# Kernel tuning notes

Measured on AMD Instinct MI355X. Metric: run time of the kernel, lower is better.

The kernel has to match this reference:

```python
import jax, jax.numpy as jnp
import numpy as np

SCALE = 1.0 / np.sqrt(7.0)  # window_size ** 0.5 with window_size=7


def setup_inputs() -> dict:
    key = jax.random.key(0)
    ks = jax.random.split(key, 7)
    B, C, H, W = 8, 64, 64, 64
    O = 64
    x = jax.random.normal(ks[0], (B, C, H, W), dtype=jnp.float32)
    s = 1.0 / np.sqrt(C)
    Wq = jax.random.normal(ks[1], (O, C), dtype=jnp.float32) * s
    bq = jax.random.normal(ks[2], (O,), dtype=jnp.float32) * 0.01
    Wk = jax.random.normal(ks[3], (O, C), dtype=jnp.float32) * s
    bk = jax.random.normal(ks[4], (O,), dtype=jnp.float32) * 0.01
    Wv = jax.random.normal(ks[5], (O, C), dtype=jnp.float32) * s
    bv = jax.random.normal(ks[6], (O,), dtype=jnp.float32) * 0.01
    return {"x": x, "Wq": Wq, "bq": bq, "Wk": Wk, "bk": bk, "Wv": Wv, "bv": bv}


def reference(x, Wq, bq, Wk, bk, Wv, bv):
    B, C, H, W = x.shape
    O = Wq.shape[0]
    N = H * W
    # 1x1 convs == per-pixel linear projections
    xf = x.reshape(B, C, N)  # [B, C, N]
    q = jnp.einsum('bcn,oc->bon', xf, Wq) + bq[None, :, None]  # [B, O, N]
    k = jnp.einsum('bcn,oc->bon', xf, Wk) + bk[None, :, None]
    v = jnp.einsum('bcn,oc->bon', xf, Wv) + bv[None, :, None]
    # global attention over all H*W positions
    attn = jnp.einsum('bcn,bcm->bnm', q, k) * SCALE  # [B, N, N]
    attn = jax.nn.softmax(attn, axis=-1)
    out = jnp.einsum('bnm,bcm->bnc', attn, v)  # [B, N, O]
    # faithful to torch's out.view(B, -1, H, W): raw row-major reshape of [B, N, O]
    return out.reshape(B, O, H, W)
```

## Files before the change

### kernel.cpp

```cpp
#include <hip/hip_runtime.h>
#include <math.h>

#define B_ 8
#define N_ 4096
#define SCALE2_ 0.54528747f

typedef __bf16 bf16x8 __attribute__((ext_vector_type(8)));
typedef float f32x4 __attribute__((ext_vector_type(4)));
typedef float f32x16 __attribute__((ext_vector_type(16)));
typedef unsigned short ushortx8 __attribute__((ext_vector_type(8)));
typedef unsigned short ushort;
typedef unsigned int uint;
typedef uint uint2v __attribute__((ext_vector_type(2)));

static __device__ __forceinline__ ushort f2bf(float f) {
  union { float f; unsigned u; } v; v.f = f;
  unsigned r = v.u + 0x7FFFu + ((v.u >> 16) & 1u);
  return (ushort)(r >> 16);
}
static __device__ __forceinline__ uint pk2(float a, float b) {
  union { __bf16 h[2]; uint u; } v;
  v.h[0] = (__bf16)a; v.h[1] = (__bf16)b;
  return v.u;
}

__global__ __launch_bounds__(256)
void proj_kernel(const float* __restrict__ x,
                 const float* __restrict__ Wq, const float* __restrict__ bq,
                 const float* __restrict__ Wk, const float* __restrict__ bk,
                 const float* __restrict__ Wv, const float* __restrict__ bv,
                 ushort* __restrict__ Qb, ushort* __restrict__ KF,
                 ushort* __restrict__ VF)
{
  __shared__ ushort sm[256][17];

  const int tid = threadIdx.x;
  const int gp  = (blockIdx.x << 8) + tid;
  const int b   = gp >> 12;
  const int y   = blockIdx.y;
  const int mat = y >> 2;
  const int o0  = (y & 3) << 4;
  const int n   = gp & 4095;

  const float* xb = x + ((size_t)b << 18) + n;
  float xr[64];
  #pragma unroll
  for (int c = 0; c < 64; ++c) xr[c] = xb[(size_t)c << 12];

  const float* W    = (mat == 0) ? Wq : (mat == 1) ? Wk : Wv;
  const float* bias = (mat == 0) ? bq : (mat == 1) ? bk : bv;

  float acc[16];
  #pragma unroll 1
  for (int j = 0; j < 16; ++j) {
    const float4* wr = (const float4*)(W + ((o0 + j) << 6));
    float a = bias[o0 + j];
    #pragma unroll
    for (int c4 = 0; c4 < 16; ++c4) {
      float4 w4 = wr[c4];
      a += w4.x * xr[4*c4] + w4.y * xr[4*c4+1] + w4.z * xr[4*c4+2] + w4.w * xr[4*c4+3];
    }
    acc[j] = a;
  }

  if (mat == 2) {
    #pragma unroll
    for (int j = 0; j < 16; ++j) sm[tid][j] = f2bf(acc[j]);
    __syncthreads();
    const int ol   = tid & 15;
    const int hh   = (tid >> 4) & 1;
    const int kvbl = tid >> 5;
    const int nb   = (blockIdx.x << 8) & 4095;
    const int kvblk = (nb >> 5) + kvbl;
    #pragma unroll
    for (int ks2 = 0; ks2 < 2; ++ks2) {
      const int kvl = (kvbl << 5) + (ks2 << 4) + (hh << 3);
      uint pk[4];
      #pragma unroll
      for (int cj = 0; cj < 8; ++cj) {
        ushort v = sm[kvl + cj][ol];
        if (cj & 1) pk[cj >> 1] |= (uint)v << 16; else pk[cj >> 1] = v;
      }
      const size_t A = ((size_t)(b * 128 + kvblk)) * 2048 + (ks2 << 10)
                     + (hh << 9) + ((o0 + ol) << 3);
      *(ushortx8*)(VF + A) = *(ushortx8*)&pk[0];
    }
  } else if (mat == 1) {
    const int ks = y & 3;
    __align__(16) ushort hv[16];
    #pragma unroll
    for (int j = 0; j < 16; ++j) hv[j] = f2bf(acc[j]);
    const size_t A0 = ((size_t)(b * 128 + (n >> 5))) * 2048 + (ks << 9)
                    + ((n & 31) << 3);
    *(ushortx8*)(KF + A0)       = *(const ushortx8*)&hv[0];
    *(ushortx8*)(KF + A0 + 256) = *(const ushortx8*)&hv[8];
  } else {
    __align__(16) ushort hv[16];
    #pragma unroll
    for (int j = 0; j < 16; ++j) hv[j] = f2bf(acc[j] * SCALE2_);
    const size_t base = ((size_t)gp << 6) + o0;
    *(ushortx8*)(Qb + base)     = *(const ushortx8*)&hv[0];
    *(ushortx8*)(Qb + base + 8) = *(const ushortx8*)&hv[8];
  }
}

__global__ __launch_bounds__(256, 3)
void flash_kernel(const ushort* __restrict__ Qb, const ushort* __restrict__ KF,
                  const ushort* __restrict__ VF, float* __restrict__ out)
{
  __shared__ float cmb[3][64][33];

  const int tid  = threadIdx.x;
  const int lane = tid & 63;
  const int w    = tid >> 6;
  const int r32  = lane & 31;
  const int h    = lane >> 5;
  const int h8   = h << 3;

  const int bidx = (blockIdx.x & 7) * 128 + (blockIdx.x >> 3);
  const int b  = bidx >> 7;
  const int qw = (bidx & 127) << 5;

  bf16x8 qf[4];
  {
    const ushort* qp = Qb + ((((size_t)b << 12) + qw + r32) << 6) + h8;
    #pragma unroll
    for (int ks = 0; ks < 4; ++ks) qf[ks] = *(const bf16x8*)(qp + (ks << 4));
  }

  const ushort* kb = KF + ((size_t)((b << 7) + (w << 5))) * 2048 + (lane << 3);
  const ushort* vb = VF + ((size_t)((b << 7) + (w << 5))) * 2048 + (h << 9) + (r32 << 3);

  const f32x16 Z = (f32x16)(0.0f);
  f32x16 acc0 = Z, acc1 = Z;
  float l_lane = 0.f;

  bf16x8 kA[4], vA[4], kB[4], vB[4];
  #define LDK(D, P) do { \
    D[0] = *(const bf16x8*)(P); \
    D[1] = *(const bf16x8*)((P) + 512); \
    D[2] = *(const bf16x8*)((P) + 1024); \
    D[3] = *(const bf16x8*)((P) + 1536); \
  } while (0)
  #define LDV(D, P) do { \
    D[0] = *(const bf16x8*)(P); \
    D[1] = *(const bf16x8*)((P) + 256); \
    D[2] = *(const bf16x8*)((P) + 1024); \
    D[3] = *(const bf16x8*)((P) + 1280); \
  } while (0)

  #define COMPUTE(KFr, VFr) do { \
    __builtin_amdgcn_s_setprio(1); \
    f32x16 s = __builtin_amdgcn_mfma_f32_32x32x16_bf16(KFr[0], qf[0], Z, 0, 0, 0); \
    s = __builtin_amdgcn_mfma_f32_32x32x16_bf16(KFr[1], qf[1], s, 0, 0, 0); \
    s = __builtin_amdgcn_mfma_f32_32x32x16_bf16(KFr[2], qf[2], s, 0, 0, 0); \
    s = __builtin_amdgcn_mfma_f32_32x32x16_bf16(KFr[3], qf[3], s, 0, 0, 0); \
    __builtin_amdgcn_s_setprio(0); \
    float rs = 0.f; \
    _Pragma("unroll") \
    for (int ii = 0; ii < 16; ++ii) { \
      float p = __builtin_exp2f(s[ii]); \
      s[ii] = p; \
      rs += p; \
    } \
    l_lane += rs; \
    bf16x8 pb0, pb1; \
    { \
      uint plo0 = pk2(s[0], s[1]); \
      uint plo1 = pk2(s[2], s[3]); \
      uint phi0 = pk2(s[4], s[5]); \
      uint phi1 = pk2(s[6], s[7]); \
      uint2v r0 = __builtin_amdgcn_permlane32_swap(plo0, phi0, false, false); \
      uint2v r1 = __builtin_amdgcn_permlane32_swap(plo1, phi1, false, false); \
      union { uint u[4]; bf16x8 v; } f_; \
      f_.u[0] = r0.x; f_.u[1] = r1.x; f_.u[2] = r0.y; f_.u[3] = r1.y; \
      pb0 = f_.v; \
    } \
    { \
      uint plo0 = pk2(s[8],  s[9]); \
      uint plo1 = pk2(s[10], s[11]); \
      uint phi0 = pk2(s[12], s[13]); \
      uint phi1 = pk2(s[14], s[15]); \
      uint2v r0 = __builtin_amdgcn_permlane32_swap(plo0, phi0, false, false); \
      uint2v r1 = __builtin_amdgcn_permlane32_swap(plo1, phi1, false, false); \
      union { uint u[4]; bf16x8 v; } f_; \
      f_.u[0] = r0.x; f_.u[1] = r1.x; f_.u[2] = r0.y; f_.u[3] = r1.y; \
      pb1 = f_.v; \
    } \
    __builtin_amdgcn_s_setprio(1); \
    acc0 = __builtin_amdgcn_mfma_f32_32x32x16_bf16(VFr[0], pb0, acc0, 0, 0, 0); \
    acc1 = __builtin_amdgcn_mfma_f32_32x32x16_bf16(VFr[1], pb0, acc1, 0, 0, 0); \
    acc0 = __builtin_amdgcn_mfma_f32_32x32x16_bf16(VFr[2], pb1, acc0, 0, 0, 0); \
    acc1 = __builtin_amdgcn_mfma_f32_32x32x16_bf16(VFr[3], pb1, acc1, 0, 0, 0); \
    __builtin_amdgcn_s_setprio(0); \
  } while (0)

  LDK(kA, kb); LDV(vA, vb);
  #pragma unroll 1
  for (int t = 0; t < 16; ++t) {
    kb += 2048; vb += 2048;
    LDK(kB, kb); LDV(vB, vb);
    COMPUTE(kA, vA);
    kb += 2048; vb += 2048;
    LDK(kA, kb); LDV(vA, vb);
    COMPUTE(kB, vB);
  }

  float l_me = l_lane + __shfl_xor(l_lane, 32);

  if (w != 0) {
    float* p = &cmb[w - 1][lane][0];
    #pragma unroll
    for (int i = 0; i < 16; ++i) { p[i] = acc0[i]; p[16 + i] = acc1[i]; }
    p[32] = l_me;
  }
  __syncthreads();
  if (w == 0) {
    float lsum = l_me;
    #pragma unroll
    for (int q = 0; q < 3; ++q) lsum += cmb[q][lane][32];
    const float inv = 1.0f / lsum;
    const size_t rowb = (((size_t)b << 12) + qw + r32) << 6;
    #pragma unroll
    for (int g = 0; g < 4; ++g) {
      f32x4 o4;
      #pragma unroll
      for (int i = 0; i < 4; ++i) {
        float v = acc0[4*g + i];
        #pragma unroll
        for (int q = 0; q < 3; ++q) v += cmb[q][lane][4*g + i];
        o4[i] = v * inv;
      }
      *(f32x4*)(out + rowb + (g << 3) + (h << 2)) = o4;
    }
    #pragma unroll
    for (int g = 0; g < 4; ++g) {
      f32x4 o4;
      #pragma unroll
      for (int i = 0; i < 4; ++i) {
        float v = acc1[4*g + i];
        #pragma unroll
        for (int q = 0; q < 3; ++q) v += cmb[q][lane][16 + 4*g + i];
        o4[i] = v * inv;
      }
      *(f32x4*)(out + rowb + 32 + (g << 3) + (h << 2)) = o4;
    }
  }
  #undef LDK
  #undef LDV
  #undef COMPUTE
}

extern "C" void kernel_launch(void* const* d_in, const int* in_sizes, int n_in,
                              void* d_out, int out_size, void* d_ws, size_t ws_size,
                              hipStream_t stream) {
  (void)in_sizes; (void)n_in; (void)out_size; (void)ws_size;
  const float* x  = (const float*)d_in[0];
  const float* Wq = (const float*)d_in[1];
  const float* bq = (const float*)d_in[2];
  const float* Wk = (const float*)d_in[3];
  const float* bk = (const float*)d_in[4];
  const float* Wv = (const float*)d_in[5];
  const float* bv = (const float*)d_in[6];
  float* out = (float*)d_out;

  const size_t SZ = (size_t)B_ * N_ * 64;
  ushort* Qb = (ushort*)d_ws;
  ushort* KF = Qb + SZ;
  ushort* VF = KF + SZ;

  proj_kernel<<<dim3(128, 12), dim3(256), 0, stream>>>(x, Wq, bq, Wk, bk, Wv, bv,
                                                       Qb, KF, VF);
  flash_kernel<<<dim3(1024), dim3(256), 0, stream>>>(Qb, KF, VF, out);
}
```

Baseline: 82.88 us.

## Process two 32-row query tiles per block to reuse K/V loads

Each flash block now handles 64 query rows (two 32-row tiles) instead of 32, so each K/V fragment loaded from global memory feeds two QK^T and PV tile computations. The grid halves to 512 blocks, occupancy target drops to 2 blocks per CU, and the combine buffer in shared memory doubles. The explicit double-buffered K/V prefetch is removed in favor of loading at the top of each iteration and relying on the two tiles' compute to hide latency. This risks exposed load latency and lower parallelism, traded for halved K/V traffic.

```diff
diff --git a/kernel.cpp b/kernel.cpp
--- a/kernel.cpp
+++ b/kernel.cpp
@@ -104,11 +104,11 @@
   }
 }
 
-__global__ __launch_bounds__(256, 3)
+__global__ __launch_bounds__(256, 2)
 void flash_kernel(const ushort* __restrict__ Qb, const ushort* __restrict__ KF,
                   const ushort* __restrict__ VF, float* __restrict__ out)
 {
-  __shared__ float cmb[3][64][33];
+  __shared__ float cmb[3][64][66];
 
   const int tid  = threadIdx.x;
   const int lane = tid & 63;
@@ -117,44 +117,34 @@
   const int h    = lane >> 5;
   const int h8   = h << 3;
 
-  const int bidx = (blockIdx.x & 7) * 128 + (blockIdx.x >> 3);
-  const int b  = bidx >> 7;
-  const int qw = (bidx & 127) << 5;
-
-  bf16x8 qf[4];
+  const int bidx = (blockIdx.x & 7) * 64 + (blockIdx.x >> 3);
+  const int b  = bidx >> 6;
+  const int qw = (bidx & 63) << 6;
+
+  bf16x8 qfA[4], qfB[4];
   {
-    const ushort* qp = Qb + ((((size_t)b << 12) + qw + r32) << 6) + h8;
-    #pragma unroll
-    for (int ks = 0; ks < 4; ++ks) qf[ks] = *(const bf16x8*)(qp + (ks << 4));
+    const ushort* qa = Qb + ((((size_t)b << 12) + qw + r32) << 6) + h8;
+    const ushort* qb2 = Qb + ((((size_t)b << 12) + qw + 32 + r32) << 6) + h8;
+    #pragma unroll
+    for (int ks = 0; ks < 4; ++ks) {
+      qfA[ks] = *(const bf16x8*)(qa + (ks << 4));
+      qfB[ks] = *(const bf16x8*)(qb2 + (ks << 4));
+    }
   }
 
   const ushort* kb = KF + ((size_t)((b << 7) + (w << 5))) * 2048 + (lane << 3);
   const ushort* vb = VF + ((size_t)((b << 7) + (w << 5))) * 2048 + (h << 9) + (r32 << 3);
 
   const f32x16 Z = (f32x16)(0.0f);
-  f32x16 acc0 = Z, acc1 = Z;
-  float l_lane = 0.f;
-
-  bf16x8 kA[4], vA[4], kB[4], vB[4];
-  #define LDK(D, P) do { \
-    D[0] = *(const bf16x8*)(P); \
-    D[1] = *(const bf16x8*)((P) + 512); \
-    D[2] = *(const bf16x8*)((P) + 1024); \
-    D[3] = *(const bf16x8*)((P) + 1536); \
-  } while (0)
-  #define LDV(D, P) do { \
-    D[0] = *(const bf16x8*)(P); \
-    D[1] = *(const bf16x8*)((P) + 256); \
-    D[2] = *(const bf16x8*)((P) + 1024); \
-    D[3] = *(const bf16x8*)((P) + 1280); \
-  } while (0)
-
-  #define COMPUTE(KFr, VFr) do { \
+  f32x16 accA0 = Z, accA1 = Z, accB0 = Z, accB1 = Z;
+  float lA = 0.f, lB = 0.f;
+
+  #define TILE(QF, A0, A1, LV) do { \
     __builtin_amdgcn_s_setprio(1); \
-    f32x16 s = __builtin_amdgcn_mfma_f32_32x32x16_bf16(KFr[0], qf[0], Z, 0, 0, 0); \
-    s = __builtin_amdgcn_mfma_f32_32x32x16_bf16(KFr[1], qf[1], s, 0, 0, 0); \
-    s = __builtin_amdgcn_mfma_f32_32x32x16_bf16(KFr[2], qf[2], s, 0, 0, 0); \
-    s = __builtin_amdgcn_mfma_f32_32x32x16_bf16(KFr[3], qf[3], s, 0, 0, 0); \
+    f32x16 s = __builtin_amdgcn_mfma_f32_32x32x16_bf16(k0, QF[0], Z, 0, 0, 0); \
+    s = __builtin_amdgcn_mfma_f32_32x32x16_bf16(k1, QF[1], s, 0, 0, 0); \
+    s = __builtin_amdgcn_mfma_f32_32x32x16_bf16(k2, QF[2], s, 0, 0, 0); \
+    s = __builtin_amdgcn_mfma_f32_32x32x16_bf16(k3, QF[3], s, 0, 0, 0); \
     __builtin_amdgcn_s_setprio(0); \
     float rs = 0.f; \
     _Pragma("unroll") \
@@ -163,7 +153,7 @@
       s[ii] = p; \
       rs += p; \
     } \
-    l_lane += rs; \
+    LV += rs; \
     bf16x8 pb0, pb1; \
     { \
       uint plo0 = pk2(s[0], s[1]); \
@@ -188,67 +178,89 @@
       pb1 = f_.v; \
     } \
     __builtin_amdgcn_s_setprio(1); \
-    acc0 = __builtin_amdgcn_mfma_f32_32x32x16_bf16(VFr[0], pb0, acc0, 0, 0, 0); \
-    acc1 = __builtin_amdgcn_mfma_f32_32x32x16_bf16(VFr[1], pb0, acc1, 0, 0, 0); \
-    acc0 = __builtin_amdgcn_mfma_f32_32x32x16_bf16(VFr[2], pb1, acc0, 0, 0, 0); \
-    acc1 = __builtin_amdgcn_mfma_f32_32x32x16_bf16(VFr[3], pb1, acc1, 0, 0, 0); \
+    A0 = __builtin_amdgcn_mfma_f32_32x32x16_bf16(v0, pb0, A0, 0, 0, 0); \
+    A1 = __builtin_amdgcn_mfma_f32_32x32x16_bf16(v1, pb0, A1, 0, 0, 0); \
+    A0 = __builtin_amdgcn_mfma_f32_32x32x16_bf16(v2, pb1, A0, 0, 0, 0); \
+    A1 = __builtin_amdgcn_mfma_f32_32x32x16_bf16(v3, pb1, A1, 0, 0, 0); \
     __builtin_amdgcn_s_setprio(0); \
   } while (0)
 
-  LDK(kA, kb); LDV(vA, vb);
   #pragma unroll 1
-  for (int t = 0; t < 16; ++t) {
+  for (int t = 0; t < 32; ++t) {
+    bf16x8 k0 = *(const bf16x8*)(kb);
+    bf16x8 k1 = *(const bf16x8*)(kb + 512);
+    bf16x8 k2 = *(const bf16x8*)(kb + 1024);
+    bf16x8 k3 = *(const bf16x8*)(kb + 1536);
+    bf16x8 v0 = *(const bf16x8*)(vb);
+    bf16x8 v1 = *(const bf16x8*)(vb + 256);
+    bf16x8 v2 = *(const bf16x8*)(vb + 1024);
+    bf16x8 v3 = *(const bf16x8*)(vb + 1280);
     kb += 2048; vb += 2048;
-    LDK(kB, kb); LDV(vB, vb);
-    COMPUTE(kA, vA);
-    kb += 2048; vb += 2048;
-    LDK(kA, kb); LDV(vA, vb);
-    COMPUTE(kB, vB);
-  }
-
-  float l_me = l_lane + __shfl_xor(l_lane, 32);
+
+    TILE(qfA, accA0, accA1, lA);
+    TILE(qfB, accB0, accB1, lB);
+  }
+  #undef TILE
+
+  float lAm = lA + __shfl_xor(lA, 32);
+  float lBm = lB + __shfl_xor(lB, 32);
 
   if (w != 0) {
     float* p = &cmb[w - 1][lane][0];
     #pragma unroll
-    for (int i = 0; i < 16; ++i) { p[i] = acc0[i]; p[16 + i] = acc1[i]; }
-    p[32] = l_me;
+    for (int i = 0; i < 16; ++i) {
+      p[i]      = accA0[i];
+      p[16 + i] = accA1[i];
+      p[32 + i] = accB0[i];
+      p[48 + i] = accB1[i];
+    }
+    p[64] = lAm;
+    p[65] = lBm;
   }
   __syncthreads();
   if (w == 0) {
-    float lsum = l_me;
-    #pragma unroll
-    for (int q = 0; q < 3; ++q) lsum += cmb[q][lane][32];
-    const float inv = 1.0f / lsum;
-    const size_t rowb = (((size_t)b << 12) + qw + r32) << 6;
+    float lsA = lAm, lsB = lBm;
+    #pragma unroll
+    for (int q = 0; q < 3; ++q) { lsA += cmb[q][lane][64]; lsB += cmb[q][lane][65]; }
+    const float invA = 1.0f / lsA;
+    const float invB = 1.0f / lsB;
+    const size_t rowA = (((size_t)b << 12) + qw + r32) << 6;
+    const size_t rowB = (((size_t)b << 12) + qw + 32 + r32) << 6;
     #pragma unroll
     for (int g = 0; g < 4; ++g) {
-      f32x4 o4;
+      f32x4 oA, oB;
       #pragma unroll
       for (int i = 0; i < 4; ++i) {
-        float v = acc0[4*g + i];
+        float vA0 = accA0[4*g + i], vB0 = accB0[4*g + i];
         #pragma unroll
-        for (int q = 0; q < 3; ++q) v += cmb[q][lane][4*g + i];
-        o4[i] = v * inv;
+        for (int q = 0; q < 3; ++q) {
+          vA0 += cmb[q][lane][4*g + i];
+          vB0 += cmb[q][lane][32 + 4*g + i];
+        }
+        oA[i] = vA0 * invA;
+        oB[i] = vB0 * invB;
       }
-      *(f32x4*)(out + rowb + (g << 3) + (h << 2)) = o4;
+      *(f32x4*)(out + rowA + (g << 3) + (h << 2)) = oA;
+      *(f32x4*)(out + rowB + (g << 3) + (h << 2)) = oB;
     }
     #pragma unroll
     for (int g = 0; g < 4; ++g) {
-      f32x4 o4;
+      f32x4 oA, oB;
       #pragma unroll
       for (int i = 0; i < 4; ++i) {
-        float v = acc1[4*g + i];
+        float vA1 = accA1[4*g + i], vB1 = accB1[4*g + i];
         #pragma unroll
-        for (int q = 0; q < 3; ++q) v += cmb[q][lane][16 + 4*g + i];
-        o4[i] = v * inv;
+        for (int q = 0; q < 3; ++q) {
+          vA1 += cmb[q][lane][16 + 4*g + i];
+          vB1 += cmb[q][lane][48 + 4*g + i];
+        }
+        oA[i] = vA1 * invA;
+        oB[i] = vB1 * invB;
       }
-      *(f32x4*)(out + rowb + 32 + (g << 3) + (h << 2)) = o4;
-    }
-  }
-  #undef LDK
-  #undef LDV
-  #undef COMPUTE
+      *(f32x4*)(out + rowA + 32 + (g << 3) + (h << 2)) = oA;
+      *(f32x4*)(out + rowB + 32 + (g << 3) + (h << 2)) = oB;
+    }
+  }
 }
 
 extern "C" void kernel_launch(void* const* d_in, const int* in_sizes, int n_in,
@@ -271,5 +283,5 @@
 
   proj_kernel<<<dim3(128, 12), dim3(256), 0, stream>>>(x, Wq, bq, Wk, bk, Wv, bv,
                                                        Qb, KF, VF);
-  flash_kernel<<<dim3(1024), dim3(256), 0, stream>>>(Qb, KF, VF, out);
-}
+  flash_kernel<<<dim3(512), dim3(256), 0, stream>>>(Qb, KF, VF, out);
+}
```

New measurement: 80.65 us (median of 2 runs). 1.03x faster.
